# Kernel optimization log

Hardware: AMD Instinct MI355X
Metric: run time of the kernel (lower is better)

## Reference

```python
import jax, jax.numpy as jnp
import numpy as np

N = 40000        # total nodes (2000 graphs x 20 nodes)
E = 60000        # edges per relation (before self-loops)
R = 6            # number of relations
IN = 32
HID = 128
OUT = 128
H = 2            # heads
C = 128          # per-head out channels (concat=False)
B = 2000         # number of graphs
NEG_SLOPE = 0.2


def setup_inputs() -> dict:
    key = jax.random.key(0)
    ks = jax.random.split(key, 16)
    rn = lambda k, s, sc=0.05: (jax.random.normal(k, s, jnp.float32) * sc)
    x = jax.random.normal(ks[0], (N, IN), jnp.float32)
    edge_index = jax.random.randint(ks[1], (R, 2, E), 0, N, dtype=jnp.int32)
    batch = (jnp.arange(N, dtype=jnp.int32) // (N // B)).astype(jnp.int32)
    return {
        "x": x, "edge_index": edge_index, "batch": batch,
        "Wl1": rn(ks[2], (R, IN, H * C)), "bl1": jnp.zeros((R, H * C), jnp.float32),
        "Wr1": rn(ks[3], (R, IN, H * C)), "br1": jnp.zeros((R, H * C), jnp.float32),
        "att1": rn(ks[4], (R, H, C)), "bias1": jnp.zeros((R, C), jnp.float32),
        "Wl2": rn(ks[5], (R, HID, H * C)), "bl2": jnp.zeros((R, H * C), jnp.float32),
        "Wr2": rn(ks[6], (R, HID, H * C)), "br2": jnp.zeros((R, H * C), jnp.float32),
        "att2": rn(ks[7], (R, H, C)), "bias2": jnp.zeros((R, C), jnp.float32),
        "ln1_g": jnp.ones((HID,), jnp.float32), "ln1_b": jnp.zeros((HID,), jnp.float32),
        "ln2_g": jnp.ones((HID,), jnp.float32), "ln2_b": jnp.zeros((HID,), jnp.float32),
        "query": rn(ks[8], (HID,), 0.02),
        "projW": rn(ks[9], (HID, OUT)), "projb": jnp.zeros((OUT,), jnp.float32),
    }


def _gatv2(x, src, dst, Wl, bl, Wr, br, att, bias):
    # x: [N, F]; src/dst: [Etot] (self-loops already appended)
    n = x.shape[0]
    xl = (x @ Wl + bl).reshape(n, H, C)   # source transform
    xr = (x @ Wr + br).reshape(n, H, C)   # target transform
    e = jax.nn.leaky_relu(xl[src] + xr[dst], NEG_SLOPE)   # [Etot, H, C]
    logits = jnp.einsum('ehc,hc->eh', e, att)             # [Etot, H]
    m = jax.ops.segment_max(logits, dst, num_segments=n)
    a = jnp.exp(logits - m[dst])
    s = jax.ops.segment_sum(a, dst, num_segments=n)
    w = a / s[dst]                                        # segment softmax
    out = jax.ops.segment_sum(w[:, :, None] * xl[src], dst, num_segments=n)
    return out.mean(axis=1) + bias                        # head-average (concat=False)


def _hetero_layer(x, edge_index, Wl, bl, Wr, br, att, bias):
    loops = jnp.broadcast_to(jnp.arange(N, dtype=edge_index.dtype), (R, N))
    src = jnp.concatenate([edge_index[:, 0, :], loops], axis=1)  # [R, E+N]
    dst = jnp.concatenate([edge_index[:, 1, :], loops], axis=1)
    outs = jax.vmap(_gatv2, in_axes=(None, 0, 0, 0, 0, 0, 0, 0, 0))(
        x, src, dst, Wl, bl, Wr, br, att, bias)
    return outs.sum(axis=0)  # HeteroConv aggr='sum'


def _layernorm(x, g, b, eps=1e-5):
    mu = x.mean(-1, keepdims=True)
    var = ((x - mu) ** 2).mean(-1, keepdims=True)
    return (x - mu) * jax.lax.rsqrt(var + eps) * g + b


def reference(x, edge_index, batch, Wl1, bl1, Wr1, br1, att1, bias1,
              Wl2, bl2, Wr2, br2, att2, bias2,
              ln1_g, ln1_b, ln2_g, ln2_b, query, projW, projb):
    h = _hetero_layer(x, edge_index, Wl1, bl1, Wr1, br1, att1, bias1)
    h = _layernorm(jnp.tanh(h), ln1_g, ln1_b)
    h = _hetero_layer(h, edge_index, Wl2, bl2, Wr2, br2, att2, bias2)
    h = _layernorm(jnp.tanh(h), ln2_g, ln2_b)
    # attention pooling over graphs (segment softmax on batch ids)
    scores = h @ query                              # [N]
    m = jax.ops.segment_max(scores, batch, num_segments=B)
    a = jnp.exp(scores - m[batch])
    s = jax.ops.segment_sum(a, batch, num_segments=B)
    w = a / s[batch]
    g = jax.ops.segment_sum(w[:, None] * h, batch, num_segments=B)  # [B, HID]
    return g @ projW + projb
```

## Files before the change

### kernel.cpp

```cpp
#include <hip/hip_runtime.h>
#include <hip/hip_bf16.h>
#include <math.h>

#define N_NODES 40000
#define E_EDGES 60000
#define R_REL 6
#define IN_F 32
#define HID_F 128
#define B_GRAPHS 2000
#define NODES_PER_G 20
#define NEG_SLOPE 0.2f
#define NB (R_REL * N_NODES)
#define NTOT (R_REL * (E_EDGES + N_NODES))
#define NBLK ((NB + 255) / 256)

typedef __bf16 bf16x8 __attribute__((ext_vector_type(8)));
typedef float f32x4 __attribute__((ext_vector_type(4)));

__device__ __forceinline__ unsigned f2bfbits(float f) {
    unsigned u = __builtin_bit_cast(unsigned, f);
    return (u + 0x7FFFu + ((u >> 16) & 1u)) >> 16;
}
__device__ __forceinline__ float bflo(unsigned u) { return __builtin_bit_cast(float, u << 16); }
__device__ __forceinline__ float bfhi(unsigned u) { return __builtin_bit_cast(float, u & 0xFFFF0000u); }

__global__ __launch_bounds__(256) void count_kernel(
    const int* __restrict__ ei, int* __restrict__ cnt)
{
    int idx = blockIdx.x * 256 + threadIdx.x;
    if (idx >= NTOT) return;
    int bin;
    if (idx < R_REL * E_EDGES) {
        int r = idx / E_EDGES, e = idx - r * E_EDGES;
        bin = r * N_NODES + ei[(size_t)r * 2 * E_EDGES + E_EDGES + e];
    } else {
        bin = idx - R_REL * E_EDGES;
    }
    atomicAdd(&cnt[bin], 1);
}

__global__ __launch_bounds__(256) void scan1_kernel(
    const int* __restrict__ cnt, int* __restrict__ part, int* __restrict__ bsum)
{
    int i = blockIdx.x * 256 + threadIdx.x;
    int v = (i < NB) ? cnt[i] : 0;
    int lane = threadIdx.x & 63, w = threadIdx.x >> 6;
    int x = v;
#pragma unroll
    for (int off = 1; off < 64; off <<= 1) {
        int y = __shfl_up(x, off, 64);
        if (lane >= off) x += y;
    }
    __shared__ int ws[4];
    if (lane == 63) ws[w] = x;
    __syncthreads();
    int add = 0;
    for (int j = 0; j < w; j++) add += ws[j];
    int incl = x + add;
    if (i < NB) part[i] = incl - v;
    if (threadIdx.x == 255) bsum[blockIdx.x] = incl;
}

__global__ __launch_bounds__(1024) void scan2_kernel(
    const int* __restrict__ bsum, int* __restrict__ boff)
{
    __shared__ int buf[1024];
    int t = threadIdx.x;
    int v0 = (t < NBLK) ? bsum[t] : 0;
    buf[t] = v0;
    __syncthreads();
    for (int off = 1; off < 1024; off <<= 1) {
        int v = (t >= off) ? buf[t - off] : 0;
        __syncthreads();
        buf[t] += v;
        __syncthreads();
    }
    if (t < NBLK) boff[t] = buf[t] - v0;
}

__global__ __launch_bounds__(256) void scan3_kernel(
    const int* __restrict__ part, const int* __restrict__ boff,
    int* __restrict__ rowptr, int* __restrict__ cursor)
{
    int i = blockIdx.x * 256 + threadIdx.x;
    if (i < NB) {
        int v = part[i] + boff[i >> 8];
        rowptr[i] = v;
        cursor[i] = v;
    }
    if (i == 0) rowptr[NB] = NTOT;
}

__global__ __launch_bounds__(256) void scatter_kernel(
    const int* __restrict__ ei, int* __restrict__ cursor, int* __restrict__ csr)
{
    int idx = blockIdx.x * 256 + threadIdx.x;
    if (idx >= NTOT) return;
    int bin, src;
    if (idx < R_REL * E_EDGES) {
        int r = idx / E_EDGES, e = idx - r * E_EDGES;
        src = ei[(size_t)r * 2 * E_EDGES + e];
        bin = r * N_NODES + ei[(size_t)r * 2 * E_EDGES + E_EDGES + e];
    } else {
        bin = idx - R_REL * E_EDGES;
        src = bin % N_NODES;
    }
    int pos = atomicAdd(&cursor[bin], 1);
    csr[pos] = src;
}

__global__ __launch_bounds__(256) void cvt_bf16_kernel(
    const float* __restrict__ src, unsigned* __restrict__ dst, int npairs)
{
    int i = blockIdx.x * 256 + threadIdx.x;
    if (i >= npairs) return;
    float2 v = *(const float2*)(src + 2 * i);
    dst[i] = f2bfbits(v.x) | (f2bfbits(v.y) << 16);
}

__global__ __launch_bounds__(256) void prep_w_kernel(
    const float* __restrict__ Wl, const float* __restrict__ Wr,
    const float* __restrict__ bl, const float* __restrict__ br,
    unsigned short* __restrict__ Bt, float* __restrict__ bcat, int K)
{
    int idx = blockIdx.x * 256 + threadIdx.x;
    if (idx >= R_REL * 512 * K) return;
    int k = idx % K;
    int rn = idx / K;
    int n = rn % 512;
    int r = rn / 512;
    int nn = n & 255;
    const float* W = (n < 256) ? Wl : Wr;
    float w = W[((size_t)r * K + k) * 256 + nn];
    Bt[idx] = (unsigned short)f2bfbits(w);
    if (k == 0)
        bcat[rn] = (n < 256) ? bl[r * 256 + nn] : br[r * 256 + nn];
}

template <int K>
__global__ __launch_bounds__(256, 2) void gemm_mfma_kernel(
    const unsigned short* __restrict__ A,
    const unsigned short* __restrict__ BtAll,
    const float* __restrict__ biasAll,
    unsigned short* __restrict__ CAll)
{
    constexpr int CH = K / 8;
    constexpr int TB = 128 * K * 2;
    __shared__ char lds[2 * TB];
    char* ldsA = lds;
    char* ldsB = lds + TB;

    int tid = threadIdx.x;
    int lane = tid & 63, wave = tid >> 6;
    int l16 = lane & 15, quad = lane >> 4;
    int wm = (wave >> 1) * 64, wn = (wave & 1) * 64;
    int ny = blockIdx.x & 3, z = blockIdx.x >> 2;
    int m0 = blockIdx.y * 128, n0 = ny * 128;

    auto SW = [](int row) { return (K == 128) ? (row & 7) : ((row >> 1) & 3); };

    const char* Bt = (const char*)(BtAll + (size_t)z * 512 * K);
#pragma unroll
    for (int it = 0; it < K / 16; ++it) {
        int s = it * 256 + tid;
        int row = s / CH, sc = s % CH;
        int c = sc ^ SW(row);
        int gr = m0 + row; gr = gr < N_NODES ? gr : N_NODES - 1;
        const char* gpA = (const char*)A + (size_t)gr * (K * 2) + c * 16;
        __builtin_amdgcn_global_load_lds(
            (const __attribute__((address_space(1))) void*)gpA,
            (__attribute__((address_space(3))) void*)(ldsA + it * 4096 + wave * 1024), 16, 0, 0);
        const char* gpB = Bt + (size_t)(n0 + row) * (K * 2) + c * 16;
        __builtin_amdgcn_global_load_lds(
            (const __attribute__((address_space(1))) void*)gpB,
            (__attribute__((address_space(3))) void*)(ldsB + it * 4096 + wave * 1024), 16, 0, 0);
    }
    __syncthreads();

    f32x4 acc[4][4];
#pragma unroll
    for (int i = 0; i < 4; i++)
#pragma unroll
        for (int j = 0; j < 4; j++) {
            acc[i][j][0] = 0.f; acc[i][j][1] = 0.f;
            acc[i][j][2] = 0.f; acc[i][j][3] = 0.f;
        }

#pragma unroll
    for (int kk = 0; kk < K / 32; ++kk) {
        bf16x8 af[4], bfr[4];
#pragma unroll
        for (int i = 0; i < 4; ++i) {
            int row = wm + i * 16 + l16;
            int slot = (kk * 4 + quad) ^ SW(row);
            af[i] = *(const bf16x8*)(ldsA + row * (K * 2) + slot * 16);
        }
#pragma unroll
        for (int j = 0; j < 4; ++j) {
            int row = wn + j * 16 + l16;
            int slot = (kk * 4 + quad) ^ SW(row);
            bfr[j] = *(const bf16x8*)(ldsB + row * (K * 2) + slot * 16);
        }
#pragma unroll
        for (int i = 0; i < 4; i++)
#pragma unroll
            for (int j = 0; j < 4; j++)
                acc[i][j] = __builtin_amdgcn_mfma_f32_16x16x32_bf16(af[i], bfr[j], acc[i][j], 0, 0, 0);
    }

    const float* bias = biasAll + z * 512;
    unsigned short* C = CAll + (size_t)z * N_NODES * 512;
    float biasj[4];
#pragma unroll
    for (int j = 0; j < 4; ++j) biasj[j] = bias[n0 + wn + j * 16 + l16];
#pragma unroll
    for (int i = 0; i < 4; i++) {
        int gr0 = m0 + wm + i * 16 + quad * 4;
#pragma unroll
        for (int j = 0; j < 4; j++) {
            int col = n0 + wn + j * 16 + l16;
#pragma unroll
            for (int rg = 0; rg < 4; rg++) {
                float a = acc[i][j][rg] + biasj[j];
                float b = __shfl_xor(a, 1);
                int grow = gr0 + rg;
                if (!(lane & 1) && grow < N_NODES) {
                    __hip_bfloat162 h2 = __float22bfloat162_rn(make_float2(a, b));
                    unsigned u;
                    __builtin_memcpy(&u, &h2, 4);
                    *(unsigned*)((char*)C + ((size_t)grow * 512 + col) * 2) = u;
                }
            }
        }
    }
}

__global__ __launch_bounds__(256) void gat6_ln_kernel(
    const unsigned short* __restrict__ XLR,
    const int* __restrict__ rowptr,
    const int* __restrict__ csr,
    const float* __restrict__ att,
    const float* __restrict__ bias,
    const float* __restrict__ lng, const float* __restrict__ lnb,
    unsigned* __restrict__ hout)
{
    int gtid = blockIdx.x * 256 + threadIdx.x;
    int d = gtid >> 6;
    int lane = threadIdx.x & 63;
    if (d >= N_NODES) return;
    int hl = lane & 31;

    float tot0 = 0.f, tot1 = 0.f, tot2 = 0.f, tot3 = 0.f;
#pragma unroll 1
    for (int r = 0; r < R_REL; r++) {
        const char* base = (const char*)XLR + (size_t)r * N_NODES * 1024;
        const unsigned* xrp = (const unsigned*)(base + (size_t)d * 1024 + 512 + lane * 8);
        unsigned xu0 = xrp[0], xu1 = xrp[1];
        float xr0 = bflo(xu0), xr1 = bfhi(xu0), xr2 = bflo(xu1), xr3 = bfhi(xu1);
        float4 av = *(const float4*)(att + r * 256 + lane * 4);

        int bin = r * N_NODES + d;
        int beg = __builtin_amdgcn_readfirstlane(rowptr[bin]);
        int end = __builtin_amdgcn_readfirstlane(rowptr[bin + 1]);

        float sA = 0.f, a0 = 0.f, a1 = 0.f, a2 = 0.f, a3 = 0.f;
        float sB = 0.f, b0 = 0.f, b1 = 0.f, b2 = 0.f, b3 = 0.f;
        int i = beg;
        for (; i + 2 <= end; i += 2) {
            int s0 = csr[i], s1 = csr[i + 1];
            const unsigned* pA = (const unsigned*)(base + (size_t)s0 * 1024 + lane * 8);
            const unsigned* pB = (const unsigned*)(base + (size_t)s1 * 1024 + lane * 8);
            unsigned uA0 = pA[0], uA1 = pA[1];
            unsigned uB0 = pB[0], uB1 = pB[1];
            float xA0 = bflo(uA0), xA1 = bfhi(uA0), xA2 = bflo(uA1), xA3 = bfhi(uA1);
            float xB0 = bflo(uB0), xB1 = bfhi(uB0), xB2 = bflo(uB1), xB3 = bfhi(uB1);
            float tA0 = xA0 + xr0, tA1 = xA1 + xr1, tA2 = xA2 + xr2, tA3 = xA3 + xr3;
            float tB0 = xB0 + xr0, tB1 = xB1 + xr1, tB2 = xB2 + xr2, tB3 = xB3 + xr3;
            tA0 = fmaxf(tA0, NEG_SLOPE * tA0); tB0 = fmaxf(tB0, NEG_SLOPE * tB0);
            tA1 = fmaxf(tA1, NEG_SLOPE * tA1); tB1 = fmaxf(tB1, NEG_SLOPE * tB1);
            tA2 = fmaxf(tA2, NEG_SLOPE * tA2); tB2 = fmaxf(tB2, NEG_SLOPE * tB2);
            tA3 = fmaxf(tA3, NEG_SLOPE * tA3); tB3 = fmaxf(tB3, NEG_SLOPE * tB3);
            float pa = tA0 * av.x + tA1 * av.y + tA2 * av.z + tA3 * av.w;
            float pb = tB0 * av.x + tB1 * av.y + tB2 * av.z + tB3 * av.w;
            pa += __shfl_xor(pa, 16); pb += __shfl_xor(pb, 16);
            pa += __shfl_xor(pa, 8);  pb += __shfl_xor(pb, 8);
            pa += __shfl_xor(pa, 4);  pb += __shfl_xor(pb, 4);
            pa += __shfl_xor(pa, 2);  pb += __shfl_xor(pb, 2);
            pa += __shfl_xor(pa, 1);  pb += __shfl_xor(pb, 1);
            float wa = __expf(fminf(pa, 60.f));
            float wb = __expf(fminf(pb, 60.f));
            sA += wa; sB += wb;
            a0 = fmaf(wa, xA0, a0); b0 = fmaf(wb, xB0, b0);
            a1 = fmaf(wa, xA1, a1); b1 = fmaf(wb, xB1, b1);
            a2 = fmaf(wa, xA2, a2); b2 = fmaf(wb, xB2, b2);
            a3 = fmaf(wa, xA3, a3); b3 = fmaf(wb, xB3, b3);
        }
        if (i < end) {
            int s0 = csr[i];
            const unsigned* pA = (const unsigned*)(base + (size_t)s0 * 1024 + lane * 8);
            unsigned uA0 = pA[0], uA1 = pA[1];
            float xA0 = bflo(uA0), xA1 = bfhi(uA0), xA2 = bflo(uA1), xA3 = bfhi(uA1);
            float tA0 = xA0 + xr0, tA1 = xA1 + xr1, tA2 = xA2 + xr2, tA3 = xA3 + xr3;
            tA0 = fmaxf(tA0, NEG_SLOPE * tA0);
            tA1 = fmaxf(tA1, NEG_SLOPE * tA1);
            tA2 = fmaxf(tA2, NEG_SLOPE * tA2);
            tA3 = fmaxf(tA3, NEG_SLOPE * tA3);
            float pa = tA0 * av.x + tA1 * av.y + tA2 * av.z + tA3 * av.w;
            pa += __shfl_xor(pa, 16);
            pa += __shfl_xor(pa, 8);
            pa += __shfl_xor(pa, 4);
            pa += __shfl_xor(pa, 2);
            pa += __shfl_xor(pa, 1);
            float wa = __expf(fminf(pa, 60.f));
            sA += wa;
            a0 = fmaf(wa, xA0, a0);
            a1 = fmaf(wa, xA1, a1);
            a2 = fmaf(wa, xA2, a2);
            a3 = fmaf(wa, xA3, a3);
        }
        sA += sB; a0 += b0; a1 += b1; a2 += b2; a3 += b3;
        float rs = 0.5f * __builtin_amdgcn_rcpf(sA);
        float o0 = a0 * rs, o1 = a1 * rs, o2 = a2 * rs, o3 = a3 * rs;
        o0 += __shfl_xor(o0, 32);
        o1 += __shfl_xor(o1, 32);
        o2 += __shfl_xor(o2, 32);
        o3 += __shfl_xor(o3, 32);
        float4 bv = *(const float4*)(bias + r * 128 + hl * 4);
        tot0 += o0 + bv.x;
        tot1 += o1 + bv.y;
        tot2 += o2 + bv.z;
        tot3 += o3 + bv.w;
    }
    float v0 = tanhf(tot0), v1 = tanhf(tot1), v2 = tanhf(tot2), v3 = tanhf(tot3);
    float sum = v0 + v1 + v2 + v3;
    float sq = v0 * v0 + v1 * v1 + v2 * v2 + v3 * v3;
#pragma unroll
    for (int off = 16; off >= 1; off >>= 1) {
        sum += __shfl_xor(sum, off);
        sq  += __shfl_xor(sq, off);
    }
    float mean = sum * (1.f / 128.f);
    float var = sq * (1.f / 128.f) - mean * mean;
    float rstd = rsqrtf(var + 1e-5f);
    float4 gg = *(const float4*)(lng + hl * 4);
    float4 bb = *(const float4*)(lnb + hl * 4);
    float o0 = (v0 - mean) * rstd * gg.x + bb.x;
    float o1 = (v1 - mean) * rstd * gg.y + bb.y;
    float o2 = (v2 - mean) * rstd * gg.z + bb.z;
    float o3 = (v3 - mean) * rstd * gg.w + bb.w;
    if (lane < 32) {
        uint2 q;
        q.x = f2bfbits(o0) | (f2bfbits(o1) << 16);
        q.y = f2bfbits(o2) | (f2bfbits(o3) << 16);
        *((uint2*)(hout + (size_t)d * 64) + hl) = q;
    }
}

__global__ __launch_bounds__(256) void pool_kernel(
    const unsigned* __restrict__ hb, const float* __restrict__ query,
    float* __restrict__ gout)
{
    int gtid = blockIdx.x * 256 + threadIdx.x;
    int bg = gtid >> 6;
    int lane = threadIdx.x & 63;
    if (bg >= B_GRAPHS) return;
    float2 q = *(const float2*)(query + 2 * lane);
    float mx = -1e30f, ssum = 0.f, g0 = 0.f, g1 = 0.f;
    for (int i = 0; i < NODES_PER_G; i++) {
        unsigned u = hb[(size_t)(bg * NODES_PER_G + i) * 64 + lane];
        float h0 = bflo(u), h1 = bfhi(u);
        float p = h0 * q.x + h1 * q.y;
#pragma unroll
        for (int off = 32; off >= 1; off >>= 1) p += __shfl_xor(p, off, 64);
        float mn = fmaxf(mx, p);
        float sc = __expf(mx - mn), w = __expf(p - mn);
        ssum = ssum * sc + w;
        g0 = g0 * sc + w * h0;
        g1 = g1 * sc + w * h1;
        mx = mn;
    }
    float2 o; o.x = g0 / ssum; o.y = g1 / ssum;
    *(float2*)(gout + (size_t)bg * 128 + 2 * lane) = o;
}

__global__ __launch_bounds__(128) void proj_kernel(
    const float* __restrict__ g, const float* __restrict__ W,
    const float* __restrict__ bias, float* __restrict__ out)
{
    int bg = blockIdx.x;
    int o = threadIdx.x;
    const float* gp = g + (size_t)bg * 128;
    float acc = bias[o];
    for (int k = 0; k < 128; k++) acc = fmaf(gp[k], W[k * 128 + o], acc);
    out[(size_t)bg * 128 + o] = acc;
}

extern "C" void kernel_launch(void* const* d_in, const int* in_sizes, int n_in,
                              void* d_out, int out_size, void* d_ws, size_t ws_size,
                              hipStream_t stream)
{
    const float* x     = (const float*)d_in[0];
    const int*   ei    = (const int*)d_in[1];
    const float* Wl1   = (const float*)d_in[3];
    const float* bl1   = (const float*)d_in[4];
    const float* Wr1   = (const float*)d_in[5];
    const float* br1   = (const float*)d_in[6];
    const float* att1  = (const float*)d_in[7];
    const float* bias1 = (const float*)d_in[8];
    const float* Wl2   = (const float*)d_in[9];
    const float* bl2   = (const float*)d_in[10];
    const float* Wr2   = (const float*)d_in[11];
    const float* br2   = (const float*)d_in[12];
    const float* att2  = (const float*)d_in[13];
    const float* bias2 = (const float*)d_in[14];
    const float* ln1g  = (const float*)d_in[15];
    const float* ln1b  = (const float*)d_in[16];
    const float* ln2g  = (const float*)d_in[17];
    const float* ln2b  = (const float*)d_in[18];
    const float* query = (const float*)d_in[19];
    const float* projW = (const float*)d_in[20];
    const float* projb = (const float*)d_in[21];
    float* out = (float*)d_out;

    unsigned short* xlr6 = (unsigned short*)d_ws;
    unsigned short* h1bf = xlr6 + (size_t)R_REL * N_NODES * 512;
    unsigned short* xbf  = h1bf + (size_t)N_NODES * 128;
    unsigned short* Bt1  = xbf + (size_t)N_NODES * 32;
    unsigned short* Bt2  = Bt1 + R_REL * 512 * 32;
    float* bc1  = (float*)(Bt2 + R_REL * 512 * 128);
    float* bc2  = bc1 + R_REL * 512;
    float* gb   = bc2 + R_REL * 512;
    int* cnt    = (int*)(gb + (size_t)B_GRAPHS * 128);
    int* part   = cnt + NB;
    int* rowptr = part + NB;
    int* cursor = rowptr + NB + 1;
    int* bsum   = cursor + NB;
    int* boff   = bsum + NBLK;
    int* csr    = boff + NBLK;

    hipMemsetAsync(cnt, 0, sizeof(int) * NB, stream);
    count_kernel<<<(NTOT + 255) / 256, 256, 0, stream>>>(ei, cnt);
    scan1_kernel<<<NBLK, 256, 0, stream>>>(cnt, part, bsum);
    scan2_kernel<<<1, 1024, 0, stream>>>(bsum, boff);
    scan3_kernel<<<NBLK, 256, 0, stream>>>(part, boff, rowptr, cursor);
    scatter_kernel<<<(NTOT + 255) / 256, 256, 0, stream>>>(ei, cursor, csr);

    cvt_bf16_kernel<<<(N_NODES * 16 + 255) / 256, 256, 0, stream>>>(x, (unsigned*)xbf, N_NODES * 16);
    prep_w_kernel<<<(R_REL * 512 * 32 + 255) / 256, 256, 0, stream>>>(Wl1, Wr1, bl1, br1, Bt1, bc1, 32);
    prep_w_kernel<<<(R_REL * 512 * 128 + 255) / 256, 256, 0, stream>>>(Wl2, Wr2, bl2, br2, Bt2, bc2, 128);

    dim3 ggrid(24, (N_NODES + 127) / 128, 1);
    gemm_mfma_kernel<32><<<ggrid, 256, 0, stream>>>(xbf, Bt1, bc1, xlr6);
    gat6_ln_kernel<<<N_NODES / 4, 256, 0, stream>>>(
        xlr6, rowptr, csr, att1, bias1, ln1g, ln1b, (unsigned*)h1bf);
    gemm_mfma_kernel<128><<<ggrid, 256, 0, stream>>>(h1bf, Bt2, bc2, xlr6);
    gat6_ln_kernel<<<N_NODES / 4, 256, 0, stream>>>(
        xlr6, rowptr, csr, att2, bias2, ln2g, ln2b, (unsigned*)h1bf);
    pool_kernel<<<B_GRAPHS / 4, 256, 0, stream>>>((unsigned*)h1bf, query, gb);
    proj_kernel<<<B_GRAPHS, 128, 0, stream>>>(gb, projW, projb, out);
}
```

Before: 472.5 us.

## Handle self-loops implicitly and prefetch per-relation rows before GAT aggregation

```diff
diff --git a/kernel.cpp b/kernel.cpp
--- a/kernel.cpp
+++ b/kernel.cpp
@@ -11,7 +11,7 @@
 #define NODES_PER_G 20
 #define NEG_SLOPE 0.2f
 #define NB (R_REL * N_NODES)
-#define NTOT (R_REL * (E_EDGES + N_NODES))
+#define NE (R_REL * E_EDGES)
 #define NBLK ((NB + 255) / 256)
 
 typedef __bf16 bf16x8 __attribute__((ext_vector_type(8)));
@@ -28,14 +28,9 @@
     const int* __restrict__ ei, int* __restrict__ cnt)
 {
     int idx = blockIdx.x * 256 + threadIdx.x;
-    if (idx >= NTOT) return;
-    int bin;
-    if (idx < R_REL * E_EDGES) {
-        int r = idx / E_EDGES, e = idx - r * E_EDGES;
-        bin = r * N_NODES + ei[(size_t)r * 2 * E_EDGES + E_EDGES + e];
-    } else {
-        bin = idx - R_REL * E_EDGES;
-    }
+    if (idx >= NE) return;
+    int r = idx / E_EDGES, e = idx - r * E_EDGES;
+    int bin = r * N_NODES + ei[(size_t)r * 2 * E_EDGES + E_EDGES + e];
     atomicAdd(&cnt[bin], 1);
 }
 
@@ -88,23 +83,17 @@
         rowptr[i] = v;
         cursor[i] = v;
     }
-    if (i == 0) rowptr[NB] = NTOT;
+    if (i == 0) rowptr[NB] = NE;
 }
 
 __global__ __launch_bounds__(256) void scatter_kernel(
     const int* __restrict__ ei, int* __restrict__ cursor, int* __restrict__ csr)
 {
     int idx = blockIdx.x * 256 + threadIdx.x;
-    if (idx >= NTOT) return;
-    int bin, src;
-    if (idx < R_REL * E_EDGES) {
-        int r = idx / E_EDGES, e = idx - r * E_EDGES;
-        src = ei[(size_t)r * 2 * E_EDGES + e];
-        bin = r * N_NODES + ei[(size_t)r * 2 * E_EDGES + E_EDGES + e];
-    } else {
-        bin = idx - R_REL * E_EDGES;
-        src = bin % N_NODES;
-    }
+    if (idx >= NE) return;
+    int r = idx / E_EDGES, e = idx - r * E_EDGES;
+    int src = ei[(size_t)r * 2 * E_EDGES + e];
+    int bin = r * N_NODES + ei[(size_t)r * 2 * E_EDGES + E_EDGES + e];
     int pos = atomicAdd(&cursor[bin], 1);
     csr[pos] = src;
 }
@@ -235,7 +224,7 @@
     }
 }
 
-__global__ __launch_bounds__(256) void gat6_ln_kernel(
+__global__ __launch_bounds__(256, 4) void gat6_ln_kernel(
     const unsigned short* __restrict__ XLR,
     const int* __restrict__ rowptr,
     const int* __restrict__ csr,
@@ -250,75 +239,116 @@
     if (d >= N_NODES) return;
     int hl = lane & 31;
 
-    float tot0 = 0.f, tot1 = 0.f, tot2 = 0.f, tot3 = 0.f;
-#pragma unroll 1
+    unsigned sd0[R_REL], sd1[R_REL];
+    unsigned rr0[R_REL], rr1[R_REL];
+    unsigned ua0[R_REL], ua1[R_REL];
+    int beg[R_REL], nn[R_REL];
+#pragma unroll
     for (int r = 0; r < R_REL; r++) {
         const char* base = (const char*)XLR + (size_t)r * N_NODES * 1024;
-        const unsigned* xrp = (const unsigned*)(base + (size_t)d * 1024 + 512 + lane * 8);
-        unsigned xu0 = xrp[0], xu1 = xrp[1];
-        float xr0 = bflo(xu0), xr1 = bfhi(xu0), xr2 = bflo(xu1), xr3 = bfhi(xu1);
+        const unsigned* p = (const unsigned*)(base + (size_t)d * 1024 + lane * 8);
+        sd0[r] = p[0];   sd1[r] = p[1];
+        rr0[r] = p[128]; rr1[r] = p[129];
+        int bin = r * N_NODES + d;
+        int b = __builtin_amdgcn_readfirstlane(rowptr[bin]);
+        int e = __builtin_amdgcn_readfirstlane(rowptr[bin + 1]);
+        beg[r] = b; nn[r] = e - b;
+        int c0 = csr[b];
+        c0 = c0 < 0 ? 0 : (c0 >= N_NODES ? N_NODES - 1 : c0);
+        const unsigned* pa = (const unsigned*)(base + (size_t)c0 * 1024 + lane * 8);
+        ua0[r] = pa[0]; ua1[r] = pa[1];
+    }
+
+    float tot0 = 0.f, tot1 = 0.f, tot2 = 0.f, tot3 = 0.f;
+#pragma unroll
+    for (int r = 0; r < R_REL; r++) {
+        const char* base = (const char*)XLR + (size_t)r * N_NODES * 1024;
+        float xr0 = bflo(rr0[r]), xr1 = bfhi(rr0[r]);
+        float xr2 = bflo(rr1[r]), xr3 = bfhi(rr1[r]);
         float4 av = *(const float4*)(att + r * 256 + lane * 4);
-
-        int bin = r * N_NODES + d;
-        int beg = __builtin_amdgcn_readfirstlane(rowptr[bin]);
-        int end = __builtin_amdgcn_readfirstlane(rowptr[bin + 1]);
-
-        float sA = 0.f, a0 = 0.f, a1 = 0.f, a2 = 0.f, a3 = 0.f;
-        float sB = 0.f, b0 = 0.f, b1 = 0.f, b2 = 0.f, b3 = 0.f;
-        int i = beg;
-        for (; i + 2 <= end; i += 2) {
-            int s0 = csr[i], s1 = csr[i + 1];
-            const unsigned* pA = (const unsigned*)(base + (size_t)s0 * 1024 + lane * 8);
-            const unsigned* pB = (const unsigned*)(base + (size_t)s1 * 1024 + lane * 8);
-            unsigned uA0 = pA[0], uA1 = pA[1];
-            unsigned uB0 = pB[0], uB1 = pB[1];
-            float xA0 = bflo(uA0), xA1 = bfhi(uA0), xA2 = bflo(uA1), xA3 = bfhi(uA1);
-            float xB0 = bflo(uB0), xB1 = bfhi(uB0), xB2 = bflo(uB1), xB3 = bfhi(uB1);
-            float tA0 = xA0 + xr0, tA1 = xA1 + xr1, tA2 = xA2 + xr2, tA3 = xA3 + xr3;
-            float tB0 = xB0 + xr0, tB1 = xB1 + xr1, tB2 = xB2 + xr2, tB3 = xB3 + xr3;
-            tA0 = fmaxf(tA0, NEG_SLOPE * tA0); tB0 = fmaxf(tB0, NEG_SLOPE * tB0);
-            tA1 = fmaxf(tA1, NEG_SLOPE * tA1); tB1 = fmaxf(tB1, NEG_SLOPE * tB1);
-            tA2 = fmaxf(tA2, NEG_SLOPE * tA2); tB2 = fmaxf(tB2, NEG_SLOPE * tB2);
-            tA3 = fmaxf(tA3, NEG_SLOPE * tA3); tB3 = fmaxf(tB3, NEG_SLOPE * tB3);
-            float pa = tA0 * av.x + tA1 * av.y + tA2 * av.z + tA3 * av.w;
-            float pb = tB0 * av.x + tB1 * av.y + tB2 * av.z + tB3 * av.w;
-            pa += __shfl_xor(pa, 16); pb += __shfl_xor(pb, 16);
-            pa += __shfl_xor(pa, 8);  pb += __shfl_xor(pb, 8);
-            pa += __shfl_xor(pa, 4);  pb += __shfl_xor(pb, 4);
-            pa += __shfl_xor(pa, 2);  pb += __shfl_xor(pb, 2);
-            pa += __shfl_xor(pa, 1);  pb += __shfl_xor(pb, 1);
-            float wa = __expf(fminf(pa, 60.f));
-            float wb = __expf(fminf(pb, 60.f));
-            sA += wa; sB += wb;
-            a0 = fmaf(wa, xA0, a0); b0 = fmaf(wb, xB0, b0);
-            a1 = fmaf(wa, xA1, a1); b1 = fmaf(wb, xB1, b1);
-            a2 = fmaf(wa, xA2, a2); b2 = fmaf(wb, xB2, b2);
-            a3 = fmaf(wa, xA3, a3); b3 = fmaf(wb, xB3, b3);
+        int n = nn[r];
+
+        float xS0 = bflo(sd0[r]), xS1 = bfhi(sd0[r]), xS2 = bflo(sd1[r]), xS3 = bfhi(sd1[r]);
+        float xA0 = bflo(ua0[r]), xA1 = bfhi(ua0[r]), xA2 = bflo(ua1[r]), xA3 = bfhi(ua1[r]);
+        float tS0 = xS0 + xr0, tS1 = xS1 + xr1, tS2 = xS2 + xr2, tS3 = xS3 + xr3;
+        float tA0 = xA0 + xr0, tA1 = xA1 + xr1, tA2 = xA2 + xr2, tA3 = xA3 + xr3;
+        tS0 = fmaxf(tS0, NEG_SLOPE * tS0); tA0 = fmaxf(tA0, NEG_SLOPE * tA0);
+        tS1 = fmaxf(tS1, NEG_SLOPE * tS1); tA1 = fmaxf(tA1, NEG_SLOPE * tA1);
+        tS2 = fmaxf(tS2, NEG_SLOPE * tS2); tA2 = fmaxf(tA2, NEG_SLOPE * tA2);
+        tS3 = fmaxf(tS3, NEG_SLOPE * tS3); tA3 = fmaxf(tA3, NEG_SLOPE * tA3);
+        float ps = tS0 * av.x + tS1 * av.y + tS2 * av.z + tS3 * av.w;
+        float pa = tA0 * av.x + tA1 * av.y + tA2 * av.z + tA3 * av.w;
+        ps += __shfl_xor(ps, 16); pa += __shfl_xor(pa, 16);
+        ps += __shfl_xor(ps, 8);  pa += __shfl_xor(pa, 8);
+        ps += __shfl_xor(ps, 4);  pa += __shfl_xor(pa, 4);
+        ps += __shfl_xor(ps, 2);  pa += __shfl_xor(pa, 2);
+        ps += __shfl_xor(ps, 1);  pa += __shfl_xor(pa, 1);
+        float wS = __expf(fminf(ps, 60.f));
+        float wA = (n >= 1) ? __expf(fminf(pa, 60.f)) : 0.f;
+        float sA = wS + wA;
+        float a0 = wS * xS0 + wA * xA0;
+        float a1 = wS * xS1 + wA * xA1;
+        float a2 = wS * xS2 + wA * xA2;
+        float a3 = wS * xS3 + wA * xA3;
+
+        if (n >= 2) {
+            float sB = 0.f, b0 = 0.f, b1 = 0.f, b2 = 0.f, b3 = 0.f;
+            int i = beg[r] + 1, end = beg[r] + n;
+            for (; i + 2 <= end; i += 2) {
+                int s0 = csr[i], s1 = csr[i + 1];
+                const unsigned* pA = (const unsigned*)(base + (size_t)s0 * 1024 + lane * 8);
+                const unsigned* pB = (const unsigned*)(base + (size_t)s1 * 1024 + lane * 8);
+                unsigned uA0 = pA[0], uA1 = pA[1];
+                unsigned uB0 = pB[0], uB1 = pB[1];
+                float yA0 = bflo(uA0), yA1 = bfhi(uA0), yA2 = bflo(uA1), yA3 = bfhi(uA1);
+                float yB0 = bflo(uB0), yB1 = bfhi(uB0), yB2 = bflo(uB1), yB3 = bfhi(uB1);
+                float uA_0 = yA0 + xr0, uA_1 = yA1 + xr1, uA_2 = yA2 + xr2, uA_3 = yA3 + xr3;
+                float uB_0 = yB0 + xr0, uB_1 = yB1 + xr1, uB_2 = yB2 + xr2, uB_3 = yB3 + xr3;
+                uA_0 = fmaxf(uA_0, NEG_SLOPE * uA_0); uB_0 = fmaxf(uB_0, NEG_SLOPE * uB_0);
+                uA_1 = fmaxf(uA_1, NEG_SLOPE * uA_1); uB_1 = fmaxf(uB_1, NEG_SLOPE * uB_1);
+                uA_2 = fmaxf(uA_2, NEG_SLOPE * uA_2); uB_2 = fmaxf(uB_2, NEG_SLOPE * uB_2);
+                uA_3 = fmaxf(uA_3, NEG_SLOPE * uA_3); uB_3 = fmaxf(uB_3, NEG_SLOPE * uB_3);
+                float qa = uA_0 * av.x + uA_1 * av.y + uA_2 * av.z + uA_3 * av.w;
+                float qb = uB_0 * av.x + uB_1 * av.y + uB_2 * av.z + uB_3 * av.w;
+                qa += __shfl_xor(qa, 16); qb += __shfl_xor(qb, 16);
+                qa += __shfl_xor(qa, 8);  qb += __shfl_xor(qb, 8);
+                qa += __shfl_xor(qa, 4);  qb += __shfl_xor(qb, 4);
+                qa += __shfl_xor(qa, 2);  qb += __shfl_xor(qb, 2);
+                qa += __shfl_xor(qa, 1);  qb += __shfl_xor(qb, 1);
+                float va = __expf(fminf(qa, 60.f));
+                float vb = __expf(fminf(qb, 60.f));
+                sA += va; sB += vb;
+                a0 = fmaf(va, yA0, a0); b0 = fmaf(vb, yB0, b0);
+                a1 = fmaf(va, yA1, a1); b1 = fmaf(vb, yB1, b1);
+                a2 = fmaf(va, yA2, a2); b2 = fmaf(vb, yB2, b2);
+                a3 = fmaf(va, yA3, a3); b3 = fmaf(vb, yB3, b3);
+            }
+            if (i < end) {
+                int s0 = csr[i];
+                const unsigned* pA = (const unsigned*)(base + (size_t)s0 * 1024 + lane * 8);
+                unsigned uA0 = pA[0], uA1 = pA[1];
+                float yA0 = bflo(uA0), yA1 = bfhi(uA0), yA2 = bflo(uA1), yA3 = bfhi(uA1);
+                float uA_0 = yA0 + xr0, uA_1 = yA1 + xr1, uA_2 = yA2 + xr2, uA_3 = yA3 + xr3;
+                uA_0 = fmaxf(uA_0, NEG_SLOPE * uA_0);
+                uA_1 = fmaxf(uA_1, NEG_SLOPE * uA_1);
+                uA_2 = fmaxf(uA_2, NEG_SLOPE * uA_2);
+                uA_3 = fmaxf(uA_3, NEG_SLOPE * uA_3);
+                float qa = uA_0 * av.x + uA_1 * av.y + uA_2 * av.z + uA_3 * av.w;
+                qa += __shfl_xor(qa, 16);
+                qa += __shfl_xor(qa, 8);
+                qa += __shfl_xor(qa, 4);
+                qa += __shfl_xor(qa, 2);
+                qa += __shfl_xor(qa, 1);
+                float va = __expf(fminf(qa, 60.f));
+                sA += va;
+                a0 = fmaf(va, yA0, a0);
+                a1 = fmaf(va, yA1, a1);
+                a2 = fmaf(va, yA2, a2);
+                a3 = fmaf(va, yA3, a3);
+            }
+            sA += sB; a0 += b0; a1 += b1; a2 += b2; a3 += b3;
         }
-        if (i < end) {
-            int s0 = csr[i];
-            const unsigned* pA = (const unsigned*)(base + (size_t)s0 * 1024 + lane * 8);
-            unsigned uA0 = pA[0], uA1 = pA[1];
-            float xA0 = bflo(uA0), xA1 = bfhi(uA0), xA2 = bflo(uA1), xA3 = bfhi(uA1);
-            float tA0 = xA0 + xr0, tA1 = xA1 + xr1, tA2 = xA2 + xr2, tA3 = xA3 + xr3;
-            tA0 = fmaxf(tA0, NEG_SLOPE * tA0);
-            tA1 = fmaxf(tA1, NEG_SLOPE * tA1);
-            tA2 = fmaxf(tA2, NEG_SLOPE * tA2);
-            tA3 = fmaxf(tA3, NEG_SLOPE * tA3);
-            float pa = tA0 * av.x + tA1 * av.y + tA2 * av.z + tA3 * av.w;
-            pa += __shfl_xor(pa, 16);
-            pa += __shfl_xor(pa, 8);
-            pa += __shfl_xor(pa, 4);
-            pa += __shfl_xor(pa, 2);
-            pa += __shfl_xor(pa, 1);
-            float wa = __expf(fminf(pa, 60.f));
-            sA += wa;
-            a0 = fmaf(wa, xA0, a0);
-            a1 = fmaf(wa, xA1, a1);
-            a2 = fmaf(wa, xA2, a2);
-            a3 = fmaf(wa, xA3, a3);
-        }
-        sA += sB; a0 += b0; a1 += b1; a2 += b2; a3 += b3;
+
         float rs = 0.5f * __builtin_amdgcn_rcpf(sA);
         float o0 = a0 * rs, o1 = a1 * rs, o2 = a2 * rs, o3 = a3 * rs;
         o0 += __shfl_xor(o0, 32);
@@ -439,11 +469,12 @@
     int* csr    = boff + NBLK;
 
     hipMemsetAsync(cnt, 0, sizeof(int) * NB, stream);
-    count_kernel<<<(NTOT + 255) / 256, 256, 0, stream>>>(ei, cnt);
+    hipMemsetAsync(csr + NE, 0, sizeof(int) * 2, stream);
+    count_kernel<<<(NE + 255) / 256, 256, 0, stream>>>(ei, cnt);
     scan1_kernel<<<NBLK, 256, 0, stream>>>(cnt, part, bsum);
     scan2_kernel<<<1, 1024, 0, stream>>>(bsum, boff);
     scan3_kernel<<<NBLK, 256, 0, stream>>>(part, boff, rowptr, cursor);
-    scatter_kernel<<<(NTOT + 255) / 256, 256, 0, stream>>>(ei, cursor, csr);
+    scatter_kernel<<<(NE + 255) / 256, 256, 0, stream>>>(ei, cursor, csr);
 
     cvt_bf16_kernel<<<(N_NODES * 16 + 255) / 256, 256, 0, stream>>>(x, (unsigned*)xbf, N_NODES * 16);
     prep_w_kernel<<<(R_REL * 512 * 32 + 255) / 256, 256, 0, stream>>>(Wl1, Wr1, bl1, br1, Bt1, bc1, 32);
```

Result: slower. 493.0 us (+4.3%).
